# Kernel optimization log

Hardware: AMD Instinct MI355X
Metric: run time of the kernel (lower is better)

## Reference

```python
import jax, jax.numpy as jnp
import numpy as np

D0 = 64      # l0 feature channels (state dim)
KC = 3       # l1 (vector) input channels (grads)
EDGE = 32    # edge embedding dim
H, DH = 4, 16
RBF = 16
MAXB = 4
SIG = 0.5
BIG = 1e9
EPS = 1e-5


def _forward(seq, xyz, aamask, num_bonds, state, grads, top_k,
             We, be, Wq, Wk, Wv0, Wv1, Wo0, Wself, b0):
    B, L, A = xyz.shape[:3]
    M = B * L * A
    x = xyz.reshape(M, 3)
    mask = aamask[seq].reshape(M)                                  # [M] bool: which atoms exist
    node0 = state.reshape(M, D0)                                   # l0 features
    l1 = jnp.transpose(grads, (1, 2, 3, 0, 4)).reshape(M, KC, 3)   # l1 (vector) features, [M,KC,3]

    # --- top-k atom graph over masked atoms (dense relaxation of make_atom_graph) ---
    d2 = jnp.sum((x[:, None, :] - x[None, :, :]) ** 2, -1)         # [M,M]
    valid = mask[:, None] & mask[None, :]
    d2m = jnp.where(valid, d2, BIG)
    ii = jnp.arange(M)
    d2m = d2m.at[ii, ii].set(BIG)                                  # exclude self-edges
    neg, idx = jax.lax.top_k(-d2m, top_k)                          # idx: [M,K] nearest masked atoms
    edge_ok = (-neg) < (BIG * 0.5)                                 # [M,K]

    rel = x[idx] - x[:, None, :]                                   # [M,K,3]
    dist = jnp.sqrt(jnp.sum(rel * rel, -1) + EPS)
    dirv = rel / dist[..., None]

    # --- edge features: distance RBF + intra-residue bond-count one-hot ---
    mus = jnp.linspace(0.0, 6.0, RBF)
    rbf = jnp.exp(-((dist[..., None] - mus) ** 2) / (2.0 * SIG * SIG))
    ri = ii // A
    ai = ii % A
    rj = idx // A
    aj = idx % A
    nbr = num_bonds[seq.reshape(-1)]                               # [B*L, A, A]
    bond = jnp.where(rj == ri[:, None], nbr[ri[:, None], ai[:, None], aj], 0)
    e = jnp.concatenate([rbf, jax.nn.one_hot(jnp.clip(bond, 0, MAXB), MAXB + 1)], -1)
    e = e @ We + be                                                # [M,K,EDGE]

    # --- SE(3)-invariant scalars from l1 features ---
    l1j = l1[idx]                                                  # [M,K,KC,3]
    inv = jnp.einsum('mkcd,mkd->mkc', l1j, dirv)                   # [M,K,KC]
    norms = jnp.sqrt(jnp.sum(l1 * l1, -1) + EPS)                   # [M,KC]

    # --- equivariant multi-head attention over neighbors ---
    kin = jnp.concatenate([node0[idx], e, inv], -1)                # [M,K,D0+EDGE+KC]
    qin = jnp.concatenate([node0, norms], -1)                      # [M,D0+KC]
    q = (qin @ Wq).reshape(M, H, DH)
    k = (kin @ Wk).reshape(M, top_k, H, DH)
    v0 = (kin @ Wv0).reshape(M, top_k, H, DH)
    v1 = (kin @ Wv1).reshape(M, top_k, H, 1 + KC)

    logits = jnp.einsum('mhd,mkhd->mhk', q, k) / float(np.sqrt(DH))
    logits = jnp.where(edge_ok[:, None, :], logits, -1e9)
    attn = jax.nn.softmax(logits, -1)                              # [M,H,K]

    o0 = jnp.einsum('mhk,mkhd->mhd', attn, v0).reshape(M, H * DH)
    out0 = o0 @ Wo0 + node0 @ Wself + b0                           # new l0 / state  [M,D0]

    coef = jnp.einsum('mhk,mkhc->mkc', attn, v1)                   # invariant coefs [M,K,1+KC]
    vmsg = coef[..., :1] * dirv + jnp.einsum('mkc,mkcd->mkd', coef[..., 1:], l1j)
    out1 = jnp.sum(vmsg, 1)                                        # l1 output shift [M,3]

    # --- scatter back through the mask (state[mask] = ...; xyz[mask] += shift/100) ---
    state_new = jnp.where(mask[:, None], out0, node0).reshape(B, L, A, D0)
    xyz_new = jnp.where(mask[:, None], x + out1 / 100.0, x).reshape(B, L, A, 3)
    return xyz_new, state_new


def setup_inputs() -> dict:
    key = jax.random.key(0)
    ks = jax.random.split(key, 16)
    B, L, A, NAA = 1, 256, 36, 21
    seq = jax.random.randint(ks[0], (B, L), 0, NAA)
    xyz = jax.random.normal(ks[1], (B, L, A, 3), jnp.float32)
    aamask = jax.random.uniform(ks[2], (NAA, A)) < 0.45
    num_bonds = jax.random.randint(ks[3], (NAA, A, A), 0, MAXB + 1)
    state = jax.random.normal(ks[4], (B, L, A, D0), jnp.float32)
    grads = jax.random.normal(ks[5], (KC, B, L, A, 3), jnp.float32)
    s = 0.05
    KIN = D0 + EDGE + KC
    QIN = D0 + KC
    We = s * jax.random.normal(ks[6], (RBF + MAXB + 1, EDGE), jnp.float32)
    be = jnp.zeros((EDGE,), jnp.float32)
    Wq = s * jax.random.normal(ks[7], (QIN, H * DH), jnp.float32)
    Wk = s * jax.random.normal(ks[8], (KIN, H * DH), jnp.float32)
    Wv0 = s * jax.random.normal(ks[9], (KIN, H * DH), jnp.float32)
    Wv1 = s * jax.random.normal(ks[10], (KIN, H * (1 + KC)), jnp.float32)
    Wo0 = s * jax.random.normal(ks[11], (H * DH, D0), jnp.float32)
    Wself = s * jax.random.normal(ks[12], (D0, D0), jnp.float32)
    b0 = jnp.zeros((D0,), jnp.float32)
    return {"seq": seq, "xyz": xyz, "aamask": aamask, "num_bonds": num_bonds,
            "state": state, "grads": grads, "top_k": 24,
            "We": We, "be": be, "Wq": Wq, "Wk": Wk, "Wv0": Wv0, "Wv1": Wv1,
            "Wo0": Wo0, "Wself": Wself, "b0": b0}


def reference(seq, xyz, aamask, num_bonds, state, grads, top_k,
              We, be, Wq, Wk, Wv0, Wv1, Wo0, Wself, b0):
    return _forward(seq, xyz, aamask, num_bonds, state, grads, top_k,
                    We, be, Wq, Wk, Wv0, Wv1, Wo0, Wself, b0)
```

## Files before the change

### kernel.cpp

```cpp
#include <hip/hip_runtime.h>
#include <math.h>

#define MTOT 9216
#define A_ 36
#define D0_ 64
#define EDGE_ 32
#define RBF_ 16
#define KNN 24
#define QIN_ 67
#define EPS_ 1e-5f

__global__ void k_prep(const int* __restrict__ seq, const float* __restrict__ xyz,
                       const int* __restrict__ aamask,
                       const float4* __restrict__ state4, float4* __restrict__ out_state4,
                       float4* __restrict__ pact, float* __restrict__ out_xyz,
                       int* __restrict__ cnt) {
    int t = blockIdx.x * blockDim.x + threadIdx.x;
    if (t < MTOT * D0_ / 4) out_state4[t] = state4[t];
    if (t < MTOT) {
        int r = t / A_;
        int a = t - r * A_;
        int mk = (aamask[seq[r] * A_ + a] != 0);
        float x0 = xyz[t * 3 + 0], x1 = xyz[t * 3 + 1], x2 = xyz[t * 3 + 2];
        out_xyz[t * 3 + 0] = x0;
        out_xyz[t * 3 + 1] = x1;
        out_xyz[t * 3 + 2] = x2;
        if (mk) {
            int p = atomicAdd(cnt, 1);
            pact[p] = make_float4(x0, x1, x2, __int_as_float(t));
        }
    }
}

#define CAPN 256
#define WPB 2
#define UNR 4
#define CHUNK (64 * UNR)

__global__ __launch_bounds__(128) void k_nbr(const float4* __restrict__ pact,
                                             const int* __restrict__ cnt,
                                             int* __restrict__ idx) {
    __shared__ uint2 s_cand[WPB][CAPN];
    __shared__ uint2 s_cand2[WPB][CAPN + 4];

    const int nact = *cnt;
    const int lane = threadIdx.x & 63;
    const int wv = threadIdx.x >> 6;
    const int slot = blockIdx.x * WPB + wv;
    if (slot >= nact) return;

    const float4 pq = pact[slot];
    const int ia = __float_as_int(pq.w);
    const unsigned long long lmask = (1ULL << lane) - 1ULL;

    auto pre = [&](float4* p, int base) {
        int b2 = (base < nact) ? base : 0;
        #pragma unroll
        for (int u = 0; u < UNR; ++u) p[u] = pact[b2 + u * 64 + lane];
    };

    unsigned cum[16];
    #pragma unroll
    for (int b = 0; b < 16; ++b) cum[b] = 0u;

    auto histo = [&](const float4* p, int base) {
        #pragma unroll
        for (int u = 0; u < UNR; ++u) {
            int c = base + u * 64 + lane;
            int j = __float_as_int(p[u].w);
            float dx = p[u].x - pq.x, dy = p[u].y - pq.y, dz = p[u].z - pq.z;
            float d2 = dx * dx + dy * dy + dz * dz;
            unsigned bt = (c < nact && j != ia) ? __float_as_uint(d2) : 0xFFFFFFFFu;
            #pragma unroll
            for (int b = 0; b < 16; ++b) {
                const unsigned L = (unsigned)(242 + 2 * b) << 22;
                cum[b] += (bt < L) ? 1u : 0u;
            }
        }
    };

    float4 pA[UNR], pB[UNR];
    pre(pA, 0);
    for (int base = 0; base < nact; base += 2 * CHUNK) {
        pre(pB, base + CHUNK);
        histo(pA, base);
        pre(pA, base + 2 * CHUNK);
        if (base + CHUNK < nact) histo(pB, base + CHUNK);
    }

    #pragma unroll
    for (int b = 0; b < 16; ++b) {
        unsigned v = cum[b];
        #pragma unroll
        for (int off = 32; off > 0; off >>= 1)
            v += (unsigned)__shfl_xor((int)v, off, 64);
        cum[b] = v;
    }

    int bsel = 15;
    #pragma unroll
    for (int b = 15; b >= 0; --b) if (cum[b] >= KNN) bsel = b;
    const unsigned limit = (unsigned)(242 + 2 * bsel) << 22;

    int nsel = 0;
    auto collect = [&](const float4* p, int base) {
        #pragma unroll
        for (int u = 0; u < UNR; ++u) {
            int c = base + u * 64 + lane;
            int j = __float_as_int(p[u].w);
            float dx = p[u].x - pq.x, dy = p[u].y - pq.y, dz = p[u].z - pq.z;
            float d2 = dx * dx + dy * dy + dz * dz;
            unsigned bits = (c < nact && j != ia) ? __float_as_uint(d2) : 0xFFFFFFFFu;
            bool sel = bits < limit;
            unsigned long long m = __ballot(sel);
            int pos = nsel + (int)__popcll(m & lmask);
            if (sel && pos < CAPN) s_cand[wv][pos] = make_uint2(bits, (unsigned)j);
            nsel += (int)__popcll(m);
        }
    };

    pre(pA, 0);
    for (int base = 0; base < nact; base += 2 * CHUNK) {
        pre(pB, base + CHUNK);
        collect(pA, base);
        pre(pA, base + 2 * CHUNK);
        if (base + CHUNK < nact) collect(pB, base + CHUNK);
    }
    __builtin_amdgcn_wave_barrier();

    const int n = min(nsel, CAPN);
    uint2 r0 = s_cand[wv][lane];
    uint2 r1 = s_cand[wv][lane + 64];
    uint2 r2 = s_cand[wv][lane + 128];
    uint2 r3 = s_cand[wv][lane + 192];
    const uint2 inval = make_uint2(0xFFFFFFFFu, 0xFFFFFFFFu);
    if (lane >= n)       r0 = inval;
    if (lane + 64 >= n)  r1 = inval;
    if (lane + 128 >= n) r2 = inval;
    if (lane + 192 >= n) r3 = inval;

    const unsigned prev = limit - (1u << 23);
    unsigned c2r[16];
    #pragma unroll
    for (int m = 0; m < 16; ++m) {
        const unsigned T = prev + ((unsigned)(m + 1) << 19);
        unsigned s = (r0.x < T) ? 1u : 0u;
        s += (r1.x < T) ? 1u : 0u;
        s += (r2.x < T) ? 1u : 0u;
        s += (r3.x < T) ? 1u : 0u;
        c2r[m] = s;
    }
    #pragma unroll
    for (int m = 0; m < 16; ++m) {
        unsigned v = c2r[m];
        #pragma unroll
        for (int off = 32; off > 0; off >>= 1)
            v += (unsigned)__shfl_xor((int)v, off, 64);
        c2r[m] = v;
    }
    int msel = 15;
    #pragma unroll
    for (int m = 15; m >= 0; --m) if (c2r[m] >= KNN) msel = m;
    const unsigned limit2 = prev + ((unsigned)(msel + 1) << 19);

    int nsel2 = 0;
    {
        #pragma unroll
        for (int t = 0; t < 4; ++t) {
            uint2 r = (t == 0) ? r0 : (t == 1) ? r1 : (t == 2) ? r2 : r3;
            bool sel = r.x < limit2;
            unsigned long long m = __ballot(sel);
            int pos = nsel2 + (int)__popcll(m & lmask);
            if (sel && pos < CAPN) s_cand2[wv][pos] = r;
            nsel2 += (int)__popcll(m);
        }
    }
    __builtin_amdgcn_wave_barrier();

    const int n2 = min(nsel2, CAPN);
    if (lane < 4) s_cand2[wv][n2 + lane] = inval;
    __builtin_amdgcn_wave_barrier();

    const int n2r = (n2 + 3) & ~3;
    for (int c = lane; c < n2; c += 64) {
        uint2 my = s_cand2[wv][c];
        int rank = 0;
        for (int c2 = 0; c2 < n2r; c2 += 4) {
            #pragma unroll
            for (int q = 0; q < 4; ++q) {
                uint2 o = s_cand2[wv][c2 + q];
                rank += (o.x < my.x || (o.x == my.x && o.y < my.y)) ? 1 : 0;
            }
        }
        if (rank < KNN) idx[ia * KNN + rank] = (int)my.y;
    }
}

#define WB() __builtin_amdgcn_wave_barrier()

__global__ __launch_bounds__(64, 2) void k_attn(
    const float* __restrict__ xyz, const int* __restrict__ seq,
    const int* __restrict__ num_bonds, const float* __restrict__ state,
    const float* __restrict__ grads,
    const float* __restrict__ We, const float* __restrict__ be,
    const float* __restrict__ Wq, const float* __restrict__ Wk,
    const float* __restrict__ Wv0, const float* __restrict__ Wv1,
    const float* __restrict__ Wo0, const float* __restrict__ Wself,
    const float* __restrict__ b0,
    const float4* __restrict__ pact, const int* __restrict__ cnt,
    const int* __restrict__ idxbuf,
    float* __restrict__ out_xyz, float* __restrict__ out_state) {
    const int nact = *cnt;
    if ((int)blockIdx.x >= nact) return;
    const int i = __float_as_int(pact[blockIdx.x].w);
    const int lane = threadIdx.x;
    const int l15 = lane & 15;
    const int h = lane >> 4;

    __shared__ float s_kin[KNN][100];
    __shared__ float s_qw[4][100];
    __shared__ float s_wkin[4][100];
    __shared__ float s_dir[KNN][4];
    __shared__ float s_rbf[KNN][RBF_];
    __shared__ float s_l1j[KNN][3][3];
    __shared__ float s_qin[68];
    __shared__ float s_q[64];
    __shared__ float s_logit[4][KNN];
    __shared__ float s_attn[4][KNN];
    __shared__ float s_o0[64];
    __shared__ float s_v1[KNN][16];
    __shared__ float s_coef[KNN][4];
    __shared__ int   s_j[KNN];
    __shared__ int   s_ok[KNN];
    __shared__ int   s_bc[KNN];
    __shared__ float s_xi[3];

    s_qin[lane] = state[i * D0_ + lane];
    if (lane < 3) {
        float g0 = grads[(lane * MTOT + i) * 3 + 0];
        float g1 = grads[(lane * MTOT + i) * 3 + 1];
        float g2 = grads[(lane * MTOT + i) * 3 + 2];
        s_qin[D0_ + lane] = sqrtf(g0 * g0 + g1 * g1 + g2 * g2 + EPS_);
        s_xi[lane] = xyz[i * 3 + lane];
    }
    if (lane < KNN) {
        int j = idxbuf[i * KNN + lane];
        int ok = (j >= 0 && j < MTOT);
        int jj = ok ? j : 0;
        s_j[lane] = jj;
        s_ok[lane] = ok;
        float dx = xyz[jj * 3 + 0] - xyz[i * 3 + 0];
        float dy = xyz[jj * 3 + 1] - xyz[i * 3 + 1];
        float dz = xyz[jj * 3 + 2] - xyz[i * 3 + 2];
        float dist = sqrtf(dx * dx + dy * dy + dz * dz + EPS_);
        s_dir[lane][0] = dx / dist;
        s_dir[lane][1] = dy / dist;
        s_dir[lane][2] = dz / dist;
        s_dir[lane][3] = dist;
        int ri = i / A_, ai = i - ri * A_;
        int rj = jj / A_, aj = jj - rj * A_;
        int b = 0;
        if (rj == ri) b = num_bonds[(seq[ri] * A_ + ai) * A_ + aj];
        s_bc[lane] = min(max(b, 0), 4);
    }
    WB();

    {
        float q0 = 0.0f, q1 = 0.0f, q2 = 0.0f, q3 = 0.0f;
        for (int c = 0; c < 64; c += 4) {
            q0 += s_qin[c + 0] * Wq[(c + 0) * 64 + lane];
            q1 += s_qin[c + 1] * Wq[(c + 1) * 64 + lane];
            q2 += s_qin[c + 2] * Wq[(c + 2) * 64 + lane];
            q3 += s_qin[c + 3] * Wq[(c + 3) * 64 + lane];
        }
        q0 += s_qin[64] * Wq[64 * 64 + lane];
        q1 += s_qin[65] * Wq[65 * 64 + lane];
        q2 += s_qin[66] * Wq[66 * 64 + lane];
        s_q[lane] = (q0 + q1) + (q2 + q3);
    }
    for (int f = lane; f < KNN * RBF_; f += 64) {
        int k = f >> 4, r = f & 15;
        float mu = (6.0f / 15.0f) * (float)r;
        float d = s_dir[k][3] - mu;
        s_rbf[k][r] = expf(-d * d * 2.0f);
    }
    for (int k = 0; k < KNN; ++k) s_kin[k][lane] = state[s_j[k] * D0_ + lane];
    for (int f = lane; f < KNN * 3; f += 64) {
        int k = f / 3, c = f - 3 * k;
        int jj = s_j[k];
        float g0 = grads[(c * MTOT + jj) * 3 + 0];
        float g1 = grads[(c * MTOT + jj) * 3 + 1];
        float g2 = grads[(c * MTOT + jj) * 3 + 2];
        s_l1j[k][c][0] = g0; s_l1j[k][c][1] = g1; s_l1j[k][c][2] = g2;
        s_kin[k][96 + c] = g0 * s_dir[k][0] + g1 * s_dir[k][1] + g2 * s_dir[k][2];
    }
    if (lane < KNN) s_kin[lane][99] = 0.0f;
    WB();

    for (int f = lane; f < KNN * EDGE_; f += 64) {
        int k = f >> 5, d = f & 31;
        float e0 = be[d] + We[(RBF_ + s_bc[k]) * EDGE_ + d];
        float e1 = 0.0f;
        #pragma unroll
        for (int r = 0; r < RBF_; r += 2) {
            e0 += s_rbf[k][r] * We[r * EDGE_ + d];
            e1 += s_rbf[k][r + 1] * We[(r + 1) * EDGE_ + d];
        }
        s_kin[k][64 + d] = e0 + e1;
    }
    for (int t = 0; t < 7; ++t) {
        int c = t * 16 + l15;
        if (c < 99) {
            const float* wk = &Wk[c * 64 + h * 16];
            float a0 = 0.0f, a1 = 0.0f;
            #pragma unroll
            for (int d = 0; d < 16; d += 2) {
                a0 += s_q[h * 16 + d] * wk[d];
                a1 += s_q[h * 16 + d + 1] * wk[d + 1];
            }
            s_qw[h][c] = a0 + a1;
        }
    }
    WB();

    for (int f = lane; f < 96; f += 64) {
        int k = f >> 2, hh = f & 3;
        const float4* k4 = (const float4*)s_kin[k];
        const float4* q4 = (const float4*)s_qw[hh];
        float a0 = 0.0f, a1 = 0.0f, a2 = 0.0f, a3 = 0.0f;
        #pragma unroll
        for (int c4 = 0; c4 < 24; c4 += 4) {
            float4 x0 = k4[c4 + 0], y0 = q4[c4 + 0];
            a0 += x0.x * y0.x + x0.y * y0.y + x0.z * y0.z + x0.w * y0.w;
            float4 x1 = k4[c4 + 1], y1 = q4[c4 + 1];
            a1 += x1.x * y1.x + x1.y * y1.y + x1.z * y1.z + x1.w * y1.w;
            float4 x2 = k4[c4 + 2], y2 = q4[c4 + 2];
            a2 += x2.x * y2.x + x2.y * y2.y + x2.z * y2.z + x2.w * y2.w;
            float4 x3 = k4[c4 + 3], y3 = q4[c4 + 3];
            a3 += x3.x * y3.x + x3.y * y3.y + x3.z * y3.z + x3.w * y3.w;
        }
        float acc = (a0 + a1) + (a2 + a3);
        acc += s_kin[k][96] * s_qw[hh][96] + s_kin[k][97] * s_qw[hh][97]
             + s_kin[k][98] * s_qw[hh][98];
        s_logit[hh][k] = s_ok[k] ? acc * 0.25f : -1e9f;
    }
    WB();

    float attn[KNN];
    {
        float mx = -1e30f;
        #pragma unroll
        for (int k = 0; k < KNN; ++k) { attn[k] = s_logit[h][k]; mx = fmaxf(mx, attn[k]); }
        float s0 = 0.0f, s1 = 0.0f, s2 = 0.0f, s3 = 0.0f;
        #pragma unroll
        for (int k = 0; k < KNN; k += 4) {
            attn[k + 0] = expf(attn[k + 0] - mx); s0 += attn[k + 0];
            attn[k + 1] = expf(attn[k + 1] - mx); s1 += attn[k + 1];
            attn[k + 2] = expf(attn[k + 2] - mx); s2 += attn[k + 2];
            attn[k + 3] = expf(attn[k + 3] - mx); s3 += attn[k + 3];
        }
        float rs = 1.0f / ((s0 + s1) + (s2 + s3));
        #pragma unroll
        for (int k = 0; k < KNN; ++k) attn[k] *= rs;
    }
    s_attn[h][l15] = attn[l15];
    if (l15 < 8) s_attn[h][16 + l15] = attn[16 + l15];

    for (int t = 0; t < 7; ++t) {
        int c = t * 16 + l15;
        if (c < 99) {
            float a0 = 0.0f, a1 = 0.0f, a2 = 0.0f, a3 = 0.0f;
            #pragma unroll
            for (int k = 0; k < KNN; k += 4) {
                a0 += attn[k + 0] * s_kin[k + 0][c];
                a1 += attn[k + 1] * s_kin[k + 1][c];
                a2 += attn[k + 2] * s_kin[k + 2][c];
                a3 += attn[k + 3] * s_kin[k + 3][c];
            }
            s_wkin[h][c] = (a0 + a1) + (a2 + a3);
        }
    }
    for (int t = 0; t < 6; ++t) {
        int k = (t * 64 + lane) >> 4;
        const float4* k4 = (const float4*)s_kin[k];
        const float* wv = &Wv1[l15];
        float a0 = 0.0f, a1 = 0.0f, a2 = 0.0f, a3 = 0.0f;
        #pragma unroll
        for (int c4 = 0; c4 < 24; c4 += 4) {
            float4 x0 = k4[c4 + 0];
            a0 += x0.x * wv[((c4 + 0) * 4 + 0) * 16] + x0.y * wv[((c4 + 0) * 4 + 1) * 16]
                + x0.z * wv[((c4 + 0) * 4 + 2) * 16] + x0.w * wv[((c4 + 0) * 4 + 3) * 16];
            float4 x1 = k4[c4 + 1];
            a1 += x1.x * wv[((c4 + 1) * 4 + 0) * 16] + x1.y * wv[((c4 + 1) * 4 + 1) * 16]
                + x1.z * wv[((c4 + 1) * 4 + 2) * 16] + x1.w * wv[((c4 + 1) * 4 + 3) * 16];
            float4 x2 = k4[c4 + 2];
            a2 += x2.x * wv[((c4 + 2) * 4 + 0) * 16] + x2.y * wv[((c4 + 2) * 4 + 1) * 16]
                + x2.z * wv[((c4 + 2) * 4 + 2) * 16] + x2.w * wv[((c4 + 2) * 4 + 3) * 16];
            float4 x3 = k4[c4 + 3];
            a3 += x3.x * wv[((c4 + 3) * 4 + 0) * 16] + x3.y * wv[((c4 + 3) * 4 + 1) * 16]
                + x3.z * wv[((c4 + 3) * 4 + 2) * 16] + x3.w * wv[((c4 + 3) * 4 + 3) * 16];
        }
        float acc = (a0 + a1) + (a2 + a3);
        acc += s_kin[k][96] * wv[96 * 16] + s_kin[k][97] * wv[97 * 16]
             + s_kin[k][98] * wv[98 * 16];
        s_v1[k][l15] = acc;
    }
    WB();

    {
        float a0 = 0.0f, a1 = 0.0f, a2 = 0.0f, a3 = 0.0f;
        for (int c = 0; c < 96; c += 4) {
            a0 += s_wkin[h][c + 0] * Wv0[(c + 0) * 64 + lane];
            a1 += s_wkin[h][c + 1] * Wv0[(c + 1) * 64 + lane];
            a2 += s_wkin[h][c + 2] * Wv0[(c + 2) * 64 + lane];
            a3 += s_wkin[h][c + 3] * Wv0[(c + 3) * 64 + lane];
        }
        a0 += s_wkin[h][96] * Wv0[96 * 64 + lane];
        a1 += s_wkin[h][97] * Wv0[97 * 64 + lane];
        a2 += s_wkin[h][98] * Wv0[98 * 64 + lane];
        s_o0[lane] = (a0 + a1) + (a2 + a3);
    }
    WB();

    {
        float a0 = b0[lane], a1 = 0.0f, a2 = 0.0f, a3 = 0.0f;
        for (int t = 0; t < 64; t += 4) {
            a0 += s_o0[t + 0] * Wo0[(t + 0) * 64 + lane];
            a1 += s_o0[t + 1] * Wo0[(t + 1) * 64 + lane];
            a2 += s_o0[t + 2] * Wo0[(t + 2) * 64 + lane];
            a3 += s_o0[t + 3] * Wo0[(t + 3) * 64 + lane];
        }
        for (int t = 0; t < 64; t += 4) {
            a0 += s_qin[t + 0] * Wself[(t + 0) * 64 + lane];
            a1 += s_qin[t + 1] * Wself[(t + 1) * 64 + lane];
            a2 += s_qin[t + 2] * Wself[(t + 2) * 64 + lane];
            a3 += s_qin[t + 3] * Wself[(t + 3) * 64 + lane];
        }
        out_state[i * D0_ + lane] = (a0 + a1) + (a2 + a3);
    }
    for (int f = lane; f < KNN * 4; f += 64) {
        int k = f >> 2, c = f & 3;
        float a2 = 0.0f;
        #pragma unroll
        for (int hh = 0; hh < 4; ++hh) a2 += s_attn[hh][k] * s_v1[k][hh * 4 + c];
        s_coef[k][c] = a2;
    }
    WB();

    if (lane < 3) {
        float o1 = 0.0f;
        #pragma unroll
        for (int k = 0; k < KNN; ++k) {
            float t = s_coef[k][0] * s_dir[k][lane];
            t += s_coef[k][1] * s_l1j[k][0][lane];
            t += s_coef[k][2] * s_l1j[k][1][lane];
            t += s_coef[k][3] * s_l1j[k][2][lane];
            o1 += t;
        }
        out_xyz[i * 3 + lane] = s_xi[lane] + o1 / 100.0f;
    }
}

extern "C" void kernel_launch(void* const* d_in, const int* in_sizes, int n_in,
                              void* d_out, int out_size, void* d_ws, size_t ws_size,
                              hipStream_t stream) {
    const int*   seq    = (const int*)d_in[0];
    const float* xyz    = (const float*)d_in[1];
    const int*   aamask = (const int*)d_in[2];
    const int*   nbonds = (const int*)d_in[3];
    const float* state  = (const float*)d_in[4];
    const float* grads  = (const float*)d_in[5];
    const float* We    = (const float*)d_in[7];
    const float* be    = (const float*)d_in[8];
    const float* Wq    = (const float*)d_in[9];
    const float* Wk    = (const float*)d_in[10];
    const float* Wv0   = (const float*)d_in[11];
    const float* Wv1   = (const float*)d_in[12];
    const float* Wo0   = (const float*)d_in[13];
    const float* Wself = (const float*)d_in[14];
    const float* b0    = (const float*)d_in[15];

    float* out_xyz   = (float*)d_out;
    float* out_state = out_xyz + MTOT * 3;

    char* ws = (char*)d_ws;
    int*    cnt  = (int*)ws;
    float4* pact = (float4*)(ws + 16);
    int*    idx  = (int*)(ws + 16 + 151552);

    hipMemsetAsync(cnt, 0, 16, stream);
    k_prep<<<(MTOT * D0_ / 4 + 255) / 256, 256, 0, stream>>>(
        seq, xyz, aamask, (const float4*)state, (float4*)out_state,
        pact, out_xyz, cnt);
    k_nbr<<<(MTOT + WPB - 1) / WPB, WPB * 64, 0, stream>>>(pact, cnt, idx);
    k_attn<<<MTOT, 64, 0, stream>>>(xyz, seq, nbonds, state, grads, We, be, Wq, Wk,
                                    Wv0, Wv1, Wo0, Wself, b0, pact, cnt, idx,
                                    out_xyz, out_state);
}
```

Before: 192.7 us.

## Alias shared buffers, fuse v1 projection with attention coef, raise occupancy

Shared-memory arrays whose lifetimes do not overlap (rbf/wkin, q/o0, logit/coef) now share union buffers, which shrinks the LDS footprint. The launch bound moves from 2 to 4 blocks per SIMD. The Wv1 projection is restructured so each lane accumulates 6 neighbors while reusing each loaded weight, and the attention-weighted coefficient is reduced with shuffles, removing the s_v1 buffer and one pass plus a barrier. Pushing for higher occupancy may cap registers and cause spills, and the 6-wide accumulation adds register pressure.

After: 280.1 us. 1.45x slower.

```diff
diff --git a/kernel.cpp b/kernel.cpp
--- a/kernel.cpp
+++ b/kernel.cpp
@@ -198,7 +198,14 @@
 
 #define WB() __builtin_amdgcn_wave_barrier()
 
-__global__ __launch_bounds__(64, 2) void k_attn(
+#define S_RBF(k, r)   s_unA[(k) * 16 + (r)]
+#define S_WKIN(hh, c) s_unA[(hh) * 100 + (c)]
+#define S_Q(t)        s_unD[t]
+#define S_O0(t)       s_unD[t]
+#define S_LOGIT(hh, k) s_unC[(hh) * 24 + (k)]
+#define S_COEF(k, c)   s_unC[(k) * 4 + (c)]
+
+__global__ __launch_bounds__(64, 4) void k_attn(
     const float* __restrict__ xyz, const int* __restrict__ seq,
     const int* __restrict__ num_bonds, const float* __restrict__ state,
     const float* __restrict__ grads,
@@ -218,18 +225,14 @@
     const int h = lane >> 4;
 
     __shared__ float s_kin[KNN][100];
+    __shared__ float s_unA[400];
     __shared__ float s_qw[4][100];
-    __shared__ float s_wkin[4][100];
+    __shared__ float s_unD[64];
+    __shared__ float s_unC[96];
     __shared__ float s_dir[KNN][4];
-    __shared__ float s_rbf[KNN][RBF_];
     __shared__ float s_l1j[KNN][3][3];
     __shared__ float s_qin[68];
-    __shared__ float s_q[64];
-    __shared__ float s_logit[4][KNN];
     __shared__ float s_attn[4][KNN];
-    __shared__ float s_o0[64];
-    __shared__ float s_v1[KNN][16];
-    __shared__ float s_coef[KNN][4];
     __shared__ int   s_j[KNN];
     __shared__ int   s_ok[KNN];
     __shared__ int   s_bc[KNN];
@@ -276,13 +279,13 @@
         q0 += s_qin[64] * Wq[64 * 64 + lane];
         q1 += s_qin[65] * Wq[65 * 64 + lane];
         q2 += s_qin[66] * Wq[66 * 64 + lane];
-        s_q[lane] = (q0 + q1) + (q2 + q3);
+        S_Q(lane) = (q0 + q1) + (q2 + q3);
     }
     for (int f = lane; f < KNN * RBF_; f += 64) {
         int k = f >> 4, r = f & 15;
         float mu = (6.0f / 15.0f) * (float)r;
         float d = s_dir[k][3] - mu;
-        s_rbf[k][r] = expf(-d * d * 2.0f);
+        S_RBF(k, r) = expf(-d * d * 2.0f);
     }
     for (int k = 0; k < KNN; ++k) s_kin[k][lane] = state[s_j[k] * D0_ + lane];
     for (int f = lane; f < KNN * 3; f += 64) {
@@ -303,8 +306,8 @@
         float e1 = 0.0f;
         #pragma unroll
         for (int r = 0; r < RBF_; r += 2) {
-            e0 += s_rbf[k][r] * We[r * EDGE_ + d];
-            e1 += s_rbf[k][r + 1] * We[(r + 1) * EDGE_ + d];
+            e0 += S_RBF(k, r) * We[r * EDGE_ + d];
+            e1 += S_RBF(k, r + 1) * We[(r + 1) * EDGE_ + d];
         }
         s_kin[k][64 + d] = e0 + e1;
     }
@@ -315,8 +318,8 @@
             float a0 = 0.0f, a1 = 0.0f;
             #pragma unroll
             for (int d = 0; d < 16; d += 2) {
-                a0 += s_q[h * 16 + d] * wk[d];
-                a1 += s_q[h * 16 + d + 1] * wk[d + 1];
+                a0 += S_Q(h * 16 + d) * wk[d];
+                a1 += S_Q(h * 16 + d + 1) * wk[d + 1];
             }
             s_qw[h][c] = a0 + a1;
         }
@@ -326,7 +329,7 @@
     for (int f = lane; f < 96; f += 64) {
         int k = f >> 2, hh = f & 3;
         const float4* k4 = (const float4*)s_kin[k];
-        const float4* q4 = (const float4*)s_qw[hh];
+        const float4* q4 = (const float4*)&s_qw[hh][0];
         float a0 = 0.0f, a1 = 0.0f, a2 = 0.0f, a3 = 0.0f;
         #pragma unroll
         for (int c4 = 0; c4 < 24; c4 += 4) {
@@ -342,7 +345,7 @@
         float acc = (a0 + a1) + (a2 + a3);
         acc += s_kin[k][96] * s_qw[hh][96] + s_kin[k][97] * s_qw[hh][97]
              + s_kin[k][98] * s_qw[hh][98];
-        s_logit[hh][k] = s_ok[k] ? acc * 0.25f : -1e9f;
+        S_LOGIT(hh, k) = s_ok[k] ? acc * 0.25f : -1e9f;
     }
     WB();
 
@@ -350,7 +353,7 @@
     {
         float mx = -1e30f;
         #pragma unroll
-        for (int k = 0; k < KNN; ++k) { attn[k] = s_logit[h][k]; mx = fmaxf(mx, attn[k]); }
+        for (int k = 0; k < KNN; ++k) { attn[k] = S_LOGIT(h, k); mx = fmaxf(mx, attn[k]); }
         float s0 = 0.0f, s1 = 0.0f, s2 = 0.0f, s3 = 0.0f;
         #pragma unroll
         for (int k = 0; k < KNN; k += 4) {
@@ -365,6 +368,7 @@
     }
     s_attn[h][l15] = attn[l15];
     if (l15 < 8) s_attn[h][16 + l15] = attn[16 + l15];
+    WB();
 
     for (int t = 0; t < 7; ++t) {
         int c = t * 16 + l15;
@@ -377,58 +381,68 @@
                 a2 += attn[k + 2] * s_kin[k + 2][c];
                 a3 += attn[k + 3] * s_kin[k + 3][c];
             }
-            s_wkin[h][c] = (a0 + a1) + (a2 + a3);
-        }
-    }
-    for (int t = 0; t < 6; ++t) {
-        int k = (t * 64 + lane) >> 4;
-        const float4* k4 = (const float4*)s_kin[k];
-        const float* wv = &Wv1[l15];
-        float a0 = 0.0f, a1 = 0.0f, a2 = 0.0f, a3 = 0.0f;
-        #pragma unroll
-        for (int c4 = 0; c4 < 24; c4 += 4) {
-            float4 x0 = k4[c4 + 0];
-            a0 += x0.x * wv[((c4 + 0) * 4 + 0) * 16] + x0.y * wv[((c4 + 0) * 4 + 1) * 16]
-                + x0.z * wv[((c4 + 0) * 4 + 2) * 16] + x0.w * wv[((c4 + 0) * 4 + 3) * 16];
-            float4 x1 = k4[c4 + 1];
-            a1 += x1.x * wv[((c4 + 1) * 4 + 0) * 16] + x1.y * wv[((c4 + 1) * 4 + 1) * 16]
-                + x1.z * wv[((c4 + 1) * 4 + 2) * 16] + x1.w * wv[((c4 + 1) * 4 + 3) * 16];
-            float4 x2 = k4[c4 + 2];
-            a2 += x2.x * wv[((c4 + 2) * 4 + 0) * 16] + x2.y * wv[((c4 + 2) * 4 + 1) * 16]
-                + x2.z * wv[((c4 + 2) * 4 + 2) * 16] + x2.w * wv[((c4 + 2) * 4 + 3) * 16];
-            float4 x3 = k4[c4 + 3];
-            a3 += x3.x * wv[((c4 + 3) * 4 + 0) * 16] + x3.y * wv[((c4 + 3) * 4 + 1) * 16]
-                + x3.z * wv[((c4 + 3) * 4 + 2) * 16] + x3.w * wv[((c4 + 3) * 4 + 3) * 16];
-        }
-        float acc = (a0 + a1) + (a2 + a3);
-        acc += s_kin[k][96] * wv[96 * 16] + s_kin[k][97] * wv[97 * 16]
-             + s_kin[k][98] * wv[98 * 16];
-        s_v1[k][l15] = acc;
+            S_WKIN(h, c) = (a0 + a1) + (a2 + a3);
+        }
+    }
+    {
+        float vacc[6];
+        #pragma unroll
+        for (int kk = 0; kk < 6; ++kk) vacc[kk] = 0.0f;
+        const float* wvb = Wv1 + l15;
+        #pragma unroll
+        for (int c4 = 0; c4 < 24; ++c4) {
+            float w0 = wvb[(c4 * 4 + 0) * 16];
+            float w1 = wvb[(c4 * 4 + 1) * 16];
+            float w2 = wvb[(c4 * 4 + 2) * 16];
+            float w3 = wvb[(c4 * 4 + 3) * 16];
+            #pragma unroll
+            for (int kk = 0; kk < 6; ++kk) {
+                float4 kv = ((const float4*)s_kin[h * 6 + kk])[c4];
+                vacc[kk] += kv.x * w0 + kv.y * w1 + kv.z * w2 + kv.w * w3;
+            }
+        }
+        {
+            float w0 = wvb[96 * 16], w1 = wvb[97 * 16], w2 = wvb[98 * 16];
+            #pragma unroll
+            for (int kk = 0; kk < 6; ++kk) {
+                float4 kv = ((const float4*)s_kin[h * 6 + kk])[24];
+                vacc[kk] += kv.x * w0 + kv.y * w1 + kv.z * w2;
+            }
+        }
+        const int hh = l15 >> 2, cu = l15 & 3;
+        #pragma unroll
+        for (int kk = 0; kk < 6; ++kk) {
+            int k = h * 6 + kk;
+            float t = s_attn[hh][k] * vacc[kk];
+            t += __shfl_xor(t, 4);
+            t += __shfl_xor(t, 8);
+            if (l15 < 4) S_COEF(k, l15) = t;
+        }
     }
     WB();
 
     {
         float a0 = 0.0f, a1 = 0.0f, a2 = 0.0f, a3 = 0.0f;
         for (int c = 0; c < 96; c += 4) {
-            a0 += s_wkin[h][c + 0] * Wv0[(c + 0) * 64 + lane];
-            a1 += s_wkin[h][c + 1] * Wv0[(c + 1) * 64 + lane];
-            a2 += s_wkin[h][c + 2] * Wv0[(c + 2) * 64 + lane];
-            a3 += s_wkin[h][c + 3] * Wv0[(c + 3) * 64 + lane];
-        }
-        a0 += s_wkin[h][96] * Wv0[96 * 64 + lane];
-        a1 += s_wkin[h][97] * Wv0[97 * 64 + lane];
-        a2 += s_wkin[h][98] * Wv0[98 * 64 + lane];
-        s_o0[lane] = (a0 + a1) + (a2 + a3);
+            a0 += S_WKIN(h, c + 0) * Wv0[(c + 0) * 64 + lane];
+            a1 += S_WKIN(h, c + 1) * Wv0[(c + 1) * 64 + lane];
+            a2 += S_WKIN(h, c + 2) * Wv0[(c + 2) * 64 + lane];
+            a3 += S_WKIN(h, c + 3) * Wv0[(c + 3) * 64 + lane];
+        }
+        a0 += S_WKIN(h, 96) * Wv0[96 * 64 + lane];
+        a1 += S_WKIN(h, 97) * Wv0[97 * 64 + lane];
+        a2 += S_WKIN(h, 98) * Wv0[98 * 64 + lane];
+        S_O0(lane) = (a0 + a1) + (a2 + a3);
     }
     WB();
 
     {
         float a0 = b0[lane], a1 = 0.0f, a2 = 0.0f, a3 = 0.0f;
         for (int t = 0; t < 64; t += 4) {
-            a0 += s_o0[t + 0] * Wo0[(t + 0) * 64 + lane];
-            a1 += s_o0[t + 1] * Wo0[(t + 1) * 64 + lane];
-            a2 += s_o0[t + 2] * Wo0[(t + 2) * 64 + lane];
-            a3 += s_o0[t + 3] * Wo0[(t + 3) * 64 + lane];
+            a0 += S_O0(t + 0) * Wo0[(t + 0) * 64 + lane];
+            a1 += S_O0(t + 1) * Wo0[(t + 1) * 64 + lane];
+            a2 += S_O0(t + 2) * Wo0[(t + 2) * 64 + lane];
+            a3 += S_O0(t + 3) * Wo0[(t + 3) * 64 + lane];
         }
         for (int t = 0; t < 64; t += 4) {
             a0 += s_qin[t + 0] * Wself[(t + 0) * 64 + lane];
@@ -438,23 +452,15 @@
         }
         out_state[i * D0_ + lane] = (a0 + a1) + (a2 + a3);
     }
-    for (int f = lane; f < KNN * 4; f += 64) {
-        int k = f >> 2, c = f & 3;
-        float a2 = 0.0f;
-        #pragma unroll
-        for (int hh = 0; hh < 4; ++hh) a2 += s_attn[hh][k] * s_v1[k][hh * 4 + c];
-        s_coef[k][c] = a2;
-    }
-    WB();
 
     if (lane < 3) {
         float o1 = 0.0f;
         #pragma unroll
         for (int k = 0; k < KNN; ++k) {
-            float t = s_coef[k][0] * s_dir[k][lane];
-            t += s_coef[k][1] * s_l1j[k][0][lane];
-            t += s_coef[k][2] * s_l1j[k][1][lane];
-            t += s_coef[k][3] * s_l1j[k][2][lane];
+            float t = S_COEF(k, 0) * s_dir[k][lane];
+            t += S_COEF(k, 1) * s_l1j[k][0][lane];
+            t += S_COEF(k, 2) * s_l1j[k][1][lane];
+            t += S_COEF(k, 3) * s_l1j[k][2][lane];
             o1 += t;
         }
         out_xyz[i * 3 + lane] = s_xi[lane] + o1 / 100.0f;
```

## Fuse top-k neighbor search into attention kernel, keep neighbors in shared memory

Applied to the files above, without the earlier changes.

Merges the neighbor-selection kernel into the attention kernel so each 64-thread block first finds its atom's 24 nearest neighbors and then runs attention on them. The neighbor indices stay in shared memory instead of going through a global buffer, which removes one kernel launch and the global write and read of the index array. In exchange the fused kernel uses more shared memory and registers per block, which may lower occupancy for both phases. The search no longer runs with two waves per block.

Result: slower. 222.0 us (+15.2%).

```diff
diff --git a/kernel.cpp b/kernel.cpp
--- a/kernel.cpp
+++ b/kernel.cpp
@@ -33,172 +33,11 @@
 }
 
 #define CAPN 256
-#define WPB 2
 #define UNR 4
 #define CHUNK (64 * UNR)
-
-__global__ __launch_bounds__(128) void k_nbr(const float4* __restrict__ pact,
-                                             const int* __restrict__ cnt,
-                                             int* __restrict__ idx) {
-    __shared__ uint2 s_cand[WPB][CAPN];
-    __shared__ uint2 s_cand2[WPB][CAPN + 4];
-
-    const int nact = *cnt;
-    const int lane = threadIdx.x & 63;
-    const int wv = threadIdx.x >> 6;
-    const int slot = blockIdx.x * WPB + wv;
-    if (slot >= nact) return;
-
-    const float4 pq = pact[slot];
-    const int ia = __float_as_int(pq.w);
-    const unsigned long long lmask = (1ULL << lane) - 1ULL;
-
-    auto pre = [&](float4* p, int base) {
-        int b2 = (base < nact) ? base : 0;
-        #pragma unroll
-        for (int u = 0; u < UNR; ++u) p[u] = pact[b2 + u * 64 + lane];
-    };
-
-    unsigned cum[16];
-    #pragma unroll
-    for (int b = 0; b < 16; ++b) cum[b] = 0u;
-
-    auto histo = [&](const float4* p, int base) {
-        #pragma unroll
-        for (int u = 0; u < UNR; ++u) {
-            int c = base + u * 64 + lane;
-            int j = __float_as_int(p[u].w);
-            float dx = p[u].x - pq.x, dy = p[u].y - pq.y, dz = p[u].z - pq.z;
-            float d2 = dx * dx + dy * dy + dz * dz;
-            unsigned bt = (c < nact && j != ia) ? __float_as_uint(d2) : 0xFFFFFFFFu;
-            #pragma unroll
-            for (int b = 0; b < 16; ++b) {
-                const unsigned L = (unsigned)(242 + 2 * b) << 22;
-                cum[b] += (bt < L) ? 1u : 0u;
-            }
-        }
-    };
-
-    float4 pA[UNR], pB[UNR];
-    pre(pA, 0);
-    for (int base = 0; base < nact; base += 2 * CHUNK) {
-        pre(pB, base + CHUNK);
-        histo(pA, base);
-        pre(pA, base + 2 * CHUNK);
-        if (base + CHUNK < nact) histo(pB, base + CHUNK);
-    }
-
-    #pragma unroll
-    for (int b = 0; b < 16; ++b) {
-        unsigned v = cum[b];
-        #pragma unroll
-        for (int off = 32; off > 0; off >>= 1)
-            v += (unsigned)__shfl_xor((int)v, off, 64);
-        cum[b] = v;
-    }
-
-    int bsel = 15;
-    #pragma unroll
-    for (int b = 15; b >= 0; --b) if (cum[b] >= KNN) bsel = b;
-    const unsigned limit = (unsigned)(242 + 2 * bsel) << 22;
-
-    int nsel = 0;
-    auto collect = [&](const float4* p, int base) {
-        #pragma unroll
-        for (int u = 0; u < UNR; ++u) {
-            int c = base + u * 64 + lane;
-            int j = __float_as_int(p[u].w);
-            float dx = p[u].x - pq.x, dy = p[u].y - pq.y, dz = p[u].z - pq.z;
-            float d2 = dx * dx + dy * dy + dz * dz;
-            unsigned bits = (c < nact && j != ia) ? __float_as_uint(d2) : 0xFFFFFFFFu;
-            bool sel = bits < limit;
-            unsigned long long m = __ballot(sel);
-            int pos = nsel + (int)__popcll(m & lmask);
-            if (sel && pos < CAPN) s_cand[wv][pos] = make_uint2(bits, (unsigned)j);
-            nsel += (int)__popcll(m);
-        }
-    };
-
-    pre(pA, 0);
-    for (int base = 0; base < nact; base += 2 * CHUNK) {
-        pre(pB, base + CHUNK);
-        collect(pA, base);
-        pre(pA, base + 2 * CHUNK);
-        if (base + CHUNK < nact) collect(pB, base + CHUNK);
-    }
-    __builtin_amdgcn_wave_barrier();
-
-    const int n = min(nsel, CAPN);
-    uint2 r0 = s_cand[wv][lane];
-    uint2 r1 = s_cand[wv][lane + 64];
-    uint2 r2 = s_cand[wv][lane + 128];
-    uint2 r3 = s_cand[wv][lane + 192];
-    const uint2 inval = make_uint2(0xFFFFFFFFu, 0xFFFFFFFFu);
-    if (lane >= n)       r0 = inval;
-    if (lane + 64 >= n)  r1 = inval;
-    if (lane + 128 >= n) r2 = inval;
-    if (lane + 192 >= n) r3 = inval;
-
-    const unsigned prev = limit - (1u << 23);
-    unsigned c2r[16];
-    #pragma unroll
-    for (int m = 0; m < 16; ++m) {
-        const unsigned T = prev + ((unsigned)(m + 1) << 19);
-        unsigned s = (r0.x < T) ? 1u : 0u;
-        s += (r1.x < T) ? 1u : 0u;
-        s += (r2.x < T) ? 1u : 0u;
-        s += (r3.x < T) ? 1u : 0u;
-        c2r[m] = s;
-    }
-    #pragma unroll
-    for (int m = 0; m < 16; ++m) {
-        unsigned v = c2r[m];
-        #pragma unroll
-        for (int off = 32; off > 0; off >>= 1)
-            v += (unsigned)__shfl_xor((int)v, off, 64);
-        c2r[m] = v;
-    }
-    int msel = 15;
-    #pragma unroll
-    for (int m = 15; m >= 0; --m) if (c2r[m] >= KNN) msel = m;
-    const unsigned limit2 = prev + ((unsigned)(msel + 1) << 19);
-
-    int nsel2 = 0;
-    {
-        #pragma unroll
-        for (int t = 0; t < 4; ++t) {
-            uint2 r = (t == 0) ? r0 : (t == 1) ? r1 : (t == 2) ? r2 : r3;
-            bool sel = r.x < limit2;
-            unsigned long long m = __ballot(sel);
-            int pos = nsel2 + (int)__popcll(m & lmask);
-            if (sel && pos < CAPN) s_cand2[wv][pos] = r;
-            nsel2 += (int)__popcll(m);
-        }
-    }
-    __builtin_amdgcn_wave_barrier();
-
-    const int n2 = min(nsel2, CAPN);
-    if (lane < 4) s_cand2[wv][n2 + lane] = inval;
-    __builtin_amdgcn_wave_barrier();
-
-    const int n2r = (n2 + 3) & ~3;
-    for (int c = lane; c < n2; c += 64) {
-        uint2 my = s_cand2[wv][c];
-        int rank = 0;
-        for (int c2 = 0; c2 < n2r; c2 += 4) {
-            #pragma unroll
-            for (int q = 0; q < 4; ++q) {
-                uint2 o = s_cand2[wv][c2 + q];
-                rank += (o.x < my.x || (o.x == my.x && o.y < my.y)) ? 1 : 0;
-            }
-        }
-        if (rank < KNN) idx[ia * KNN + rank] = (int)my.y;
-    }
-}
-
 #define WB() __builtin_amdgcn_wave_barrier()
 
-__global__ __launch_bounds__(64, 2) void k_attn(
+__global__ __launch_bounds__(64, 2) void k_fused(
     const float* __restrict__ xyz, const int* __restrict__ seq,
     const int* __restrict__ num_bonds, const float* __restrict__ state,
     const float* __restrict__ grads,
@@ -208,14 +47,11 @@
     const float* __restrict__ Wo0, const float* __restrict__ Wself,
     const float* __restrict__ b0,
     const float4* __restrict__ pact, const int* __restrict__ cnt,
-    const int* __restrict__ idxbuf,
     float* __restrict__ out_xyz, float* __restrict__ out_state) {
-    const int nact = *cnt;
-    if ((int)blockIdx.x >= nact) return;
-    const int i = __float_as_int(pact[blockIdx.x].w);
-    const int lane = threadIdx.x;
-    const int l15 = lane & 15;
-    const int h = lane >> 4;
+
+    __shared__ uint2 s_cand[CAPN];
+    __shared__ uint2 s_cand2[CAPN + 4];
+    __shared__ int   s_nbr[KNN];
 
     __shared__ float s_kin[KNN][100];
     __shared__ float s_qw[4][100];
@@ -235,6 +71,164 @@
     __shared__ int   s_bc[KNN];
     __shared__ float s_xi[3];
 
+    const int nact = *cnt;
+    const int lane = threadIdx.x;
+    const int slot = blockIdx.x;
+    if (slot >= nact) return;
+
+    const float4 pq = pact[slot];
+    const int ia = __float_as_int(pq.w);
+    const unsigned long long lmask = (1ULL << lane) - 1ULL;
+
+    if (lane < KNN) s_nbr[lane] = -1;
+
+    auto pre = [&](float4* p, int base) {
+        int b2 = (base < nact) ? base : 0;
+        #pragma unroll
+        for (int u = 0; u < UNR; ++u) p[u] = pact[b2 + u * 64 + lane];
+    };
+
+    unsigned cum[16];
+    #pragma unroll
+    for (int b = 0; b < 16; ++b) cum[b] = 0u;
+
+    auto histo = [&](const float4* p, int base) {
+        #pragma unroll
+        for (int u = 0; u < UNR; ++u) {
+            int c = base + u * 64 + lane;
+            int j = __float_as_int(p[u].w);
+            float dx = p[u].x - pq.x, dy = p[u].y - pq.y, dz = p[u].z - pq.z;
+            float d2 = dx * dx + dy * dy + dz * dz;
+            unsigned bt = (c < nact && j != ia) ? __float_as_uint(d2) : 0xFFFFFFFFu;
+            #pragma unroll
+            for (int b = 0; b < 16; ++b) {
+                const unsigned L = (unsigned)(242 + 2 * b) << 22;
+                cum[b] += (bt < L) ? 1u : 0u;
+            }
+        }
+    };
+
+    float4 pA[UNR], pB[UNR];
+    pre(pA, 0);
+    for (int base = 0; base < nact; base += 2 * CHUNK) {
+        pre(pB, base + CHUNK);
+        histo(pA, base);
+        pre(pA, base + 2 * CHUNK);
+        if (base + CHUNK < nact) histo(pB, base + CHUNK);
+    }
+
+    #pragma unroll
+    for (int b = 0; b < 16; ++b) {
+        unsigned v = cum[b];
+        #pragma unroll
+        for (int off = 32; off > 0; off >>= 1)
+            v += (unsigned)__shfl_xor((int)v, off, 64);
+        cum[b] = v;
+    }
+
+    int bsel = 15;
+    #pragma unroll
+    for (int b = 15; b >= 0; --b) if (cum[b] >= KNN) bsel = b;
+    const unsigned limit = (unsigned)(242 + 2 * bsel) << 22;
+
+    int nsel = 0;
+    auto collect = [&](const float4* p, int base) {
+        #pragma unroll
+        for (int u = 0; u < UNR; ++u) {
+            int c = base + u * 64 + lane;
+            int j = __float_as_int(p[u].w);
+            float dx = p[u].x - pq.x, dy = p[u].y - pq.y, dz = p[u].z - pq.z;
+            float d2 = dx * dx + dy * dy + dz * dz;
+            unsigned bits = (c < nact && j != ia) ? __float_as_uint(d2) : 0xFFFFFFFFu;
+            bool sel = bits < limit;
+            unsigned long long m = __ballot(sel);
+            int pos = nsel + (int)__popcll(m & lmask);
+            if (sel && pos < CAPN) s_cand[pos] = make_uint2(bits, (unsigned)j);
+            nsel += (int)__popcll(m);
+        }
+    };
+
+    pre(pA, 0);
+    for (int base = 0; base < nact; base += 2 * CHUNK) {
+        pre(pB, base + CHUNK);
+        collect(pA, base);
+        pre(pA, base + 2 * CHUNK);
+        if (base + CHUNK < nact) collect(pB, base + CHUNK);
+    }
+    WB();
+
+    const int n = min(nsel, CAPN);
+    uint2 r0 = s_cand[lane];
+    uint2 r1 = s_cand[lane + 64];
+    uint2 r2 = s_cand[lane + 128];
+    uint2 r3 = s_cand[lane + 192];
+    const uint2 inval = make_uint2(0xFFFFFFFFu, 0xFFFFFFFFu);
+    if (lane >= n)       r0 = inval;
+    if (lane + 64 >= n)  r1 = inval;
+    if (lane + 128 >= n) r2 = inval;
+    if (lane + 192 >= n) r3 = inval;
+
+    const unsigned prev = limit - (1u << 23);
+    unsigned c2r[16];
+    #pragma unroll
+    for (int m = 0; m < 16; ++m) {
+        const unsigned T = prev + ((unsigned)(m + 1) << 19);
+        unsigned s = (r0.x < T) ? 1u : 0u;
+        s += (r1.x < T) ? 1u : 0u;
+        s += (r2.x < T) ? 1u : 0u;
+        s += (r3.x < T) ? 1u : 0u;
+        c2r[m] = s;
+    }
+    #pragma unroll
+    for (int m = 0; m < 16; ++m) {
+        unsigned v = c2r[m];
+        #pragma unroll
+        for (int off = 32; off > 0; off >>= 1)
+            v += (unsigned)__shfl_xor((int)v, off, 64);
+        c2r[m] = v;
+    }
+    int msel = 15;
+    #pragma unroll
+    for (int m = 15; m >= 0; --m) if (c2r[m] >= KNN) msel = m;
+    const unsigned limit2 = prev + ((unsigned)(msel + 1) << 19);
+
+    int nsel2 = 0;
+    {
+        #pragma unroll
+        for (int t = 0; t < 4; ++t) {
+            uint2 r = (t == 0) ? r0 : (t == 1) ? r1 : (t == 2) ? r2 : r3;
+            bool sel = r.x < limit2;
+            unsigned long long m = __ballot(sel);
+            int pos = nsel2 + (int)__popcll(m & lmask);
+            if (sel && pos < CAPN) s_cand2[pos] = r;
+            nsel2 += (int)__popcll(m);
+        }
+    }
+    WB();
+
+    const int n2 = min(nsel2, CAPN);
+    if (lane < 4) s_cand2[n2 + lane] = inval;
+    WB();
+
+    const int n2r = (n2 + 3) & ~3;
+    for (int c = lane; c < n2; c += 64) {
+        uint2 my = s_cand2[c];
+        int rank = 0;
+        for (int c2 = 0; c2 < n2r; c2 += 4) {
+            #pragma unroll
+            for (int q = 0; q < 4; ++q) {
+                uint2 o = s_cand2[c2 + q];
+                rank += (o.x < my.x || (o.x == my.x && o.y < my.y)) ? 1 : 0;
+            }
+        }
+        if (rank < KNN) s_nbr[rank] = (int)my.y;
+    }
+    WB();
+
+    const int i = ia;
+    const int l15 = lane & 15;
+    const int h = lane >> 4;
+
     s_qin[lane] = state[i * D0_ + lane];
     if (lane < 3) {
         float g0 = grads[(lane * MTOT + i) * 3 + 0];
@@ -244,7 +238,7 @@
         s_xi[lane] = xyz[i * 3 + lane];
     }
     if (lane < KNN) {
-        int j = idxbuf[i * KNN + lane];
+        int j = s_nbr[lane];
         int ok = (j >= 0 && j < MTOT);
         int jj = ok ? j : 0;
         s_j[lane] = jj;
@@ -486,14 +480,12 @@
     char* ws = (char*)d_ws;
     int*    cnt  = (int*)ws;
     float4* pact = (float4*)(ws + 16);
-    int*    idx  = (int*)(ws + 16 + 151552);
 
     hipMemsetAsync(cnt, 0, 16, stream);
     k_prep<<<(MTOT * D0_ / 4 + 255) / 256, 256, 0, stream>>>(
         seq, xyz, aamask, (const float4*)state, (float4*)out_state,
         pact, out_xyz, cnt);
-    k_nbr<<<(MTOT + WPB - 1) / WPB, WPB * 64, 0, stream>>>(pact, cnt, idx);
-    k_attn<<<MTOT, 64, 0, stream>>>(xyz, seq, nbonds, state, grads, We, be, Wq, Wk,
-                                    Wv0, Wv1, Wo0, Wself, b0, pact, cnt, idx,
-                                    out_xyz, out_state);
+    k_fused<<<MTOT, 64, 0, stream>>>(xyz, seq, nbonds, state, grads, We, be, Wq, Wk,
+                                     Wv0, Wv1, Wo0, Wself, b0, pact, cnt,
+                                     out_xyz, out_state);
 }
```
